# Performance work log

Hardware: AMD Instinct MI355X
Metric: run time of the kernel (lower is better)

The kernel has to match this reference:

```python
import jax, jax.numpy as jnp
import numpy as np

B, S, H = 1024, 512, 768
D1, D2 = 128, 1


def setup_inputs() -> dict:
    key = jax.random.key(0)
    k_feat, k_start, k_len, k_w1, k_w2 = jax.random.split(key, 5)
    features_extract = jax.random.normal(k_feat, (B, S, H), dtype=jnp.float32)
    start_token_idx = jax.random.randint(k_start, (B,), 1, 200, dtype=jnp.int64)
    span_len = jax.random.randint(k_len, (B,), 1, 65, dtype=jnp.int64)
    end_token_idx = start_token_idx + span_len  # guaranteed start < end <= 264 < S
    W1 = jax.random.normal(k_w1, (2 * H, D1), dtype=jnp.float32) * (1.0 / np.sqrt(2 * H))
    b1 = jnp.zeros((D1,), dtype=jnp.float32)
    W2 = jax.random.normal(k_w2, (D1, D2), dtype=jnp.float32) * (1.0 / np.sqrt(D1))
    b2 = jnp.zeros((D2,), dtype=jnp.float32)
    return {
        "features_extract": features_extract,
        "start_token_idx": start_token_idx,
        "end_token_idx": end_token_idx,
        "W1": W1, "b1": b1, "W2": W2, "b2": b2,
    }


def reference(features_extract, start_token_idx, end_token_idx, W1, b1, W2, b2):
    # CLS feature: token 0 of each example -> [B, 1, H]
    features_cls = features_extract[:, 0, :][:, None, :]

    # Ragged span mean-pool (vectorized replacement for the per-example loop):
    # mask[b, s] = start[b] <= s < end[b]
    pos = jnp.arange(features_extract.shape[1])  # [S]
    mask = (pos[None, :] >= start_token_idx[:, None]) & (pos[None, :] < end_token_idx[:, None])
    maskf = mask.astype(features_extract.dtype)  # [B, S]
    span_sum = jnp.einsum('bsh,bs->bh', features_extract, maskf)
    span_len = (end_token_idx - start_token_idx).astype(features_extract.dtype)  # >= 1
    features_crc = (span_sum / span_len[:, None])[:, None, :]  # [B, 1, H]

    # Concat + MLP head (dropout layers are identity in eval)
    features = jnp.concatenate([features_cls, features_crc], axis=2)  # [B, 1, 2H]
    h = jax.nn.relu(jnp.einsum('bid,dk->bik', features, W1) + b1)
    out = jax.nn.sigmoid(jnp.einsum('bik,ko->bio', h, W2) + b2)  # [B, 1, 1]
    return out
```

## Files before the change

kernel.cpp:

```cpp
#include <hip/hip_runtime.h>
#include <math.h>

constexpr int Bn = 1024;
constexpr int S  = 512;
constexpr int H  = 768;
constexpr int D1 = 128;
constexpr int HV = H / 4;
constexpr int K2 = 2 * H;
constexpr int NK = K2 / 32;
constexpr int NKH = 24;
constexpr int NCAST = 8;
constexpr int NCLS = 128;

typedef _Float16 half8 __attribute__((ext_vector_type(8)));
typedef _Float16 half4v __attribute__((ext_vector_type(4)));
typedef float floatx4 __attribute__((ext_vector_type(4)));


__device__ __forceinline__ size_t swz_off(int tile, int kk, int lg, int idx) {
  return ((((size_t)tile * NK + kk) * 64) + lg * 16 + idx) * 8;
}

__global__ __launch_bounds__(256) void launch1(
    const float* __restrict__ feat, const int* __restrict__ start,
    const int* __restrict__ endp, const float* __restrict__ W1,
    _Float16* __restrict__ gcrc, _Float16* __restrict__ w1s,
    float* __restrict__ p0) {
  __shared__ float4 pacc[4][3][64];
  const int t = threadIdx.x;

  if (blockIdx.x < NCAST) {
    const int c  = blockIdx.x + 8;
    const int n  = t & 127;
    const int sb = t >> 7;
    const int nt = n >> 4, ni = n & 15;
    #pragma unroll
    for (int j = 0; j < 6; ++j) {
      const int k0 = c * 96 + sb * 48 + j * 8;
      _Float16 h[8];
      #pragma unroll
      for (int i = 0; i < 8; ++i) {
        h[i] = (_Float16)W1[(size_t)(k0 + i) * D1 + n];
      }
      const int kk = k0 >> 5, lg = (k0 >> 3) & 3;
      *reinterpret_cast<half8*>(w1s + swz_off(nt, kk, lg, ni)) =
          *reinterpret_cast<half8*>(h);
    }
    return;
  }

  if (blockIdx.x < NCAST + NCLS) {
    const int w = t >> 6, l = t & 63;
    const int tid = (blockIdx.x - NCAST) * 4 + w;
    const int eg = tid & 63;
    const int nt = tid >> 6;
    const int lg = l >> 4, li = l & 15;
    const int e0 = eg * 16;
    const int n = nt * 16 + li;

    const float* arow = feat + (size_t)(e0 + li) * S * H;
    const float* wcol = W1 + n;

    floatx4 acc0 = {0.f, 0.f, 0.f, 0.f};
    floatx4 acc1 = {0.f, 0.f, 0.f, 0.f};
    #pragma unroll 2
    for (int kk = 0; kk < NKH; kk += 2) {
      #define MKFRAG(kkq, accq)                                            \
      {                                                                    \
        const int kb = (kkq) * 32 + lg * 8;                                \
        float4 fa = *reinterpret_cast<const float4*>(arow + kb);           \
        float4 fb = *reinterpret_cast<const float4*>(arow + kb + 4);       \
        const float* wb = wcol + (size_t)kb * D1;                          \
        float w0 = wb[0 * D1], w1v = wb[1 * D1], w2v = wb[2 * D1];         \
        float w3v = wb[3 * D1], w4v = wb[4 * D1], w5v = wb[5 * D1];        \
        float w6v = wb[6 * D1], w7v = wb[7 * D1];                          \
        half8 av, bv;                                                      \
        av[0] = (_Float16)fa.x; av[1] = (_Float16)fa.y;                    \
        av[2] = (_Float16)fa.z; av[3] = (_Float16)fa.w;                    \
        av[4] = (_Float16)fb.x; av[5] = (_Float16)fb.y;                    \
        av[6] = (_Float16)fb.z; av[7] = (_Float16)fb.w;                    \
        bv[0] = (_Float16)w0;  bv[1] = (_Float16)w1v;                      \
        bv[2] = (_Float16)w2v; bv[3] = (_Float16)w3v;                      \
        bv[4] = (_Float16)w4v; bv[5] = (_Float16)w5v;                      \
        bv[6] = (_Float16)w6v; bv[7] = (_Float16)w7v;                      \
        accq = __builtin_amdgcn_mfma_f32_16x16x32_f16(av, bv, accq, 0, 0, 0); \
      }
      MKFRAG(kk, acc0)
      MKFRAG(kk + 1, acc1)
      #undef MKFRAG
    }
    #pragma unroll
    for (int r = 0; r < 4; ++r) {
      p0[(size_t)(e0 + lg * 4 + r) * D1 + n] = acc0[r] + acc1[r];
    }
    return;
  }

  const int b = blockIdx.x - (NCAST + NCLS);
  const int w = t >> 6;
  const int l = t & 63;
  const float4* base =
      reinterpret_cast<const float4*>(feat) + (size_t)b * (S * HV);

  const int s0 = start[b];
  const int s1 = endp[b];

  float4 c0{0,0,0,0}, c1{0,0,0,0}, c2{0,0,0,0};
  float4 d0{0,0,0,0}, d1{0,0,0,0}, d2{0,0,0,0};
  int s = s0 + w;
  for (; s + 4 < s1; s += 8) {
    const float4* r0 = base + (size_t)s * HV;
    const float4* r1 = base + (size_t)(s + 4) * HV;
    float4 u0 = r0[l], u1 = r0[l + 64], u2 = r0[l + 128];
    float4 v0 = r1[l], v1 = r1[l + 64], v2 = r1[l + 128];
    c0.x += u0.x; c0.y += u0.y; c0.z += u0.z; c0.w += u0.w;
    c1.x += u1.x; c1.y += u1.y; c1.z += u1.z; c1.w += u1.w;
    c2.x += u2.x; c2.y += u2.y; c2.z += u2.z; c2.w += u2.w;
    d0.x += v0.x; d0.y += v0.y; d0.z += v0.z; d0.w += v0.w;
    d1.x += v1.x; d1.y += v1.y; d1.z += v1.z; d1.w += v1.w;
    d2.x += v2.x; d2.y += v2.y; d2.z += v2.z; d2.w += v2.w;
  }
  for (; s < s1; s += 4) {
    const float4* r0 = base + (size_t)s * HV;
    float4 u0 = r0[l], u1 = r0[l + 64], u2 = r0[l + 128];
    c0.x += u0.x; c0.y += u0.y; c0.z += u0.z; c0.w += u0.w;
    c1.x += u1.x; c1.y += u1.y; c1.z += u1.z; c1.w += u1.w;
    c2.x += u2.x; c2.y += u2.y; c2.z += u2.z; c2.w += u2.w;
  }
  c0.x += d0.x; c0.y += d0.y; c0.z += d0.z; c0.w += d0.w;
  c1.x += d1.x; c1.y += d1.y; c1.z += d1.z; c1.w += d1.w;
  c2.x += d2.x; c2.y += d2.y; c2.z += d2.z; c2.w += d2.w;
  pacc[w][0][l] = c0;
  pacc[w][1][l] = c1;
  pacc[w][2][l] = c2;
  __syncthreads();

  if (t < 192) {
    const int seg = t >> 6, ln = t & 63;
    float4 a = pacc[0][seg][ln], bb = pacc[1][seg][ln];
    float4 cq = pacc[2][seg][ln], dq = pacc[3][seg][ln];
    const float inv = 1.0f / (float)(s1 - s0);
    half4v r;
    r.x = (_Float16)(((a.x + bb.x) + (cq.x + dq.x)) * inv);
    r.y = (_Float16)(((a.y + bb.y) + (cq.y + dq.y)) * inv);
    r.z = (_Float16)(((a.z + bb.z) + (cq.z + dq.z)) * inv);
    r.w = (_Float16)(((a.w + bb.w) + (cq.w + dq.w)) * inv);
    *reinterpret_cast<half4v*>(gcrc + (size_t)b * H + t * 4) = r;
  }
}

__global__ __launch_bounds__(64) void crc_mfma(
    const _Float16* __restrict__ gcrc, const _Float16* __restrict__ w1s,
    float* __restrict__ p1, float* __restrict__ p2) {
  const int l  = threadIdx.x;
  const int eg = blockIdx.x & 63;
  const int rest = blockIdx.x >> 6;
  const int nt = rest >> 1;
  const int kq = rest & 1;

  const int lg = l >> 4, li = l & 15;
  const int e0 = eg * 16;

  const _Float16* Abase = gcrc + (size_t)(e0 + li) * H + kq * 384 + lg * 8;
  const half8* Bp = reinterpret_cast<const half8*>(w1s) +
                    ((size_t)nt * NK + NKH + kq * 12) * 64 + l;

  floatx4 acc0 = {0.f, 0.f, 0.f, 0.f};
  floatx4 acc1 = {0.f, 0.f, 0.f, 0.f};
  #pragma unroll 3
  for (int kk = 0; kk < 12; kk += 4) {
    half8 a0 = *reinterpret_cast<const half8*>(Abase + (kk + 0) * 32);
    half8 b0 = Bp[(size_t)(kk + 0) * 64];
    half8 a1 = *reinterpret_cast<const half8*>(Abase + (kk + 1) * 32);
    half8 b1v = Bp[(size_t)(kk + 1) * 64];
    half8 a2 = *reinterpret_cast<const half8*>(Abase + (kk + 2) * 32);
    half8 b2v = Bp[(size_t)(kk + 2) * 64];
    half8 a3 = *reinterpret_cast<const half8*>(Abase + (kk + 3) * 32);
    half8 b3v = Bp[(size_t)(kk + 3) * 64];
    acc0 = __builtin_amdgcn_mfma_f32_16x16x32_f16(a0, b0, acc0, 0, 0, 0);
    acc1 = __builtin_amdgcn_mfma_f32_16x16x32_f16(a1, b1v, acc1, 0, 0, 0);
    acc0 = __builtin_amdgcn_mfma_f32_16x16x32_f16(a2, b2v, acc0, 0, 0, 0);
    acc1 = __builtin_amdgcn_mfma_f32_16x16x32_f16(a3, b3v, acc1, 0, 0, 0);
  }

  float* plane = kq ? p2 : p1;
  const int n = nt * 16 + li;
  #pragma unroll
  for (int r = 0; r < 4; ++r) {
    plane[(size_t)(e0 + lg * 4 + r) * D1 + n] = acc0[r] + acc1[r];
  }
}

__global__ __launch_bounds__(256) void fin(
    const float* __restrict__ p0, const float* __restrict__ p1,
    const float* __restrict__ p2, const float* __restrict__ b1,
    const float* __restrict__ W2, const float* __restrict__ b2,
    float* __restrict__ out) {
  const int t = threadIdx.x;
  const int w = t >> 6, l = t & 63;
  const int e = blockIdx.x * 4 + w;
  const int k0 = l, k1 = l + 64;
  const size_t base = (size_t)e * D1;
  float h0 = b1[k0] + p0[base + k0] + p1[base + k0] + p2[base + k0];
  float h1 = b1[k1] + p0[base + k1] + p1[base + k1] + p2[base + k1];
  h0 = fmaxf(h0, 0.f); h1 = fmaxf(h1, 0.f);
  float v = h0 * W2[k0] + h1 * W2[k1];
  #pragma unroll
  for (int off = 32; off > 0; off >>= 1) v += __shfl_down(v, off);
  if (l == 0) out[e] = 1.0f / (1.0f + expf(-(v + b2[0])));
}

extern "C" void kernel_launch(void* const* d_in, const int* in_sizes, int n_in,
                              void* d_out, int out_size, void* d_ws, size_t ws_size,
                              hipStream_t stream) {
  const float* feat = (const float*)d_in[0];
  const int* start  = (const int*)d_in[1];
  const int* endp   = (const int*)d_in[2];
  const float* W1   = (const float*)d_in[3];
  const float* b1   = (const float*)d_in[4];
  const float* W2   = (const float*)d_in[5];
  const float* b2   = (const float*)d_in[6];
  float* out = (float*)d_out;

  _Float16* gcrc = (_Float16*)d_ws;
  _Float16* w1s  = gcrc + (size_t)Bn * H;
  float* p0 = (float*)(w1s + (size_t)D1 * K2);
  float* p1 = p0 + (size_t)Bn * D1;
  float* p2 = p1 + (size_t)Bn * D1;

  hipLaunchKernelGGL(launch1, dim3(NCAST + NCLS + Bn), dim3(256), 0, stream,
                     feat, start, endp, W1, gcrc, w1s, p0);
  hipLaunchKernelGGL(crc_mfma, dim3(1024), dim3(64), 0, stream,
                     gcrc, w1s, p1, p2);
  hipLaunchKernelGGL(fin, dim3(Bn / 4), dim3(256), 0, stream,
                     p0, p1, p2, b1, W2, b2, out);
}
```

Measured before the change: 30.59 us.

## Fuse CRC MFMA GEMM with MLP finish into one kernel via shared memory

Merges the crc_mfma GEMM kernel and the fin epilogue kernel into a single 1024-thread kernel per 16-example group. The 16 waves each compute one (n-tile, k-half) partial and write it to shared memory, then each wave reduces one example's hidden vector, applies ReLU, the W2 dot product and the sigmoid. This removes one kernel launch and the global round-trip of the p1/p2 partial planes. In exchange only 64 blocks are launched, which lowers parallelism compared with the previous 1024 small blocks.

```diff
diff --git a/kernel.cpp b/kernel.cpp
--- a/kernel.cpp
+++ b/kernel.cpp
@@ -149,17 +149,21 @@
   }
 }
 
-__global__ __launch_bounds__(64) void crc_mfma(
+__global__ __launch_bounds__(1024) void crc_fin(
     const _Float16* __restrict__ gcrc, const _Float16* __restrict__ w1s,
-    float* __restrict__ p1, float* __restrict__ p2) {
-  const int l  = threadIdx.x;
-  const int eg = blockIdx.x & 63;
-  const int rest = blockIdx.x >> 6;
-  const int nt = rest >> 1;
-  const int kq = rest & 1;
-
+    const float* __restrict__ p0, const float* __restrict__ b1,
+    const float* __restrict__ W2, const float* __restrict__ b2,
+    float* __restrict__ out) {
+  __shared__ float part[16][16][16];
+
+  const int t = threadIdx.x;
+  const int w = t >> 6;
+  const int l = t & 63;
+  const int eg = blockIdx.x;
+  const int e0 = eg * 16;
+  const int nt = w >> 1;
+  const int kq = w & 1;
   const int lg = l >> 4, li = l & 15;
-  const int e0 = eg * 16;
 
   const _Float16* Abase = gcrc + (size_t)(e0 + li) * H + kq * 384 + lg * 8;
   const half8* Bp = reinterpret_cast<const half8*>(w1s) +
@@ -183,31 +187,27 @@
     acc1 = __builtin_amdgcn_mfma_f32_16x16x32_f16(a3, b3v, acc1, 0, 0, 0);
   }
 
-  float* plane = kq ? p2 : p1;
-  const int n = nt * 16 + li;
   #pragma unroll
   for (int r = 0; r < 4; ++r) {
-    plane[(size_t)(e0 + lg * 4 + r) * D1 + n] = acc0[r] + acc1[r];
-  }
-}
-
-__global__ __launch_bounds__(256) void fin(
-    const float* __restrict__ p0, const float* __restrict__ p1,
-    const float* __restrict__ p2, const float* __restrict__ b1,
-    const float* __restrict__ W2, const float* __restrict__ b2,
-    float* __restrict__ out) {
-  const int t = threadIdx.x;
-  const int w = t >> 6, l = t & 63;
-  const int e = blockIdx.x * 4 + w;
-  const int k0 = l, k1 = l + 64;
-  const size_t base = (size_t)e * D1;
-  float h0 = b1[k0] + p0[base + k0] + p1[base + k0] + p2[base + k0];
-  float h1 = b1[k1] + p0[base + k1] + p1[base + k1] + p2[base + k1];
-  h0 = fmaxf(h0, 0.f); h1 = fmaxf(h1, 0.f);
-  float v = h0 * W2[k0] + h1 * W2[k1];
-  #pragma unroll
-  for (int off = 32; off > 0; off >>= 1) v += __shfl_down(v, off);
-  if (l == 0) out[e] = 1.0f / (1.0f + expf(-(v + b2[0])));
+    part[w][lg * 4 + r][li] = acc0[r] + acc1[r];
+  }
+  __syncthreads();
+
+  {
+    const int e = e0 + w;
+    const int n0 = l, n1 = l + 64;
+    const int nl = l & 15;
+    const int t0 = (l >> 4) * 2;
+    const int t1 = t0 + 8;
+    const size_t pb = (size_t)e * D1;
+    float h0 = b1[n0] + p0[pb + n0] + part[t0][w][nl] + part[t0 + 1][w][nl];
+    float h1 = b1[n1] + p0[pb + n1] + part[t1][w][nl] + part[t1 + 1][w][nl];
+    h0 = fmaxf(h0, 0.f); h1 = fmaxf(h1, 0.f);
+    float v = h0 * W2[n0] + h1 * W2[n1];
+    #pragma unroll
+    for (int off = 32; off > 0; off >>= 1) v += __shfl_down(v, off);
+    if (l == 0) out[e] = 1.0f / (1.0f + expf(-(v + b2[0])));
+  }
 }
 
 extern "C" void kernel_launch(void* const* d_in, const int* in_sizes, int n_in,
@@ -225,13 +225,9 @@
   _Float16* gcrc = (_Float16*)d_ws;
   _Float16* w1s  = gcrc + (size_t)Bn * H;
   float* p0 = (float*)(w1s + (size_t)D1 * K2);
-  float* p1 = p0 + (size_t)Bn * D1;
-  float* p2 = p1 + (size_t)Bn * D1;
 
   hipLaunchKernelGGL(launch1, dim3(NCAST + NCLS + Bn), dim3(256), 0, stream,
                      feat, start, endp, W1, gcrc, w1s, p0);
-  hipLaunchKernelGGL(crc_mfma, dim3(1024), dim3(64), 0, stream,
-                     gcrc, w1s, p1, p2);
-  hipLaunchKernelGGL(fin, dim3(Bn / 4), dim3(256), 0, stream,
-                     p0, p1, p2, b1, W2, b2, out);
-}
+  hipLaunchKernelGGL(crc_fin, dim3(64), dim3(1024), 0, stream,
+                     gcrc, w1s, p0, b1, W2, b2, out);
+}
```

Result: slower. 34.10 us (+11.5%).
